# Optimization experiments

Hardware: AMD Instinct MI355X
Metric: run time of the kernel (lower is better)

Reference implementation:

```python
import jax, jax.numpy as jnp
import numpy as np

N_HEADS = 16
HEAD_DIM = 64  # dim=1024 / n_heads=16


def setup_inputs() -> dict:
    key = jax.random.key(0)
    ks = jax.random.split(key, 7)
    B, S, D = 4, 2048, 1024
    scale = 1.0 / np.sqrt(D)
    return {
        "q": jax.random.normal(ks[0], (B, S, D), jnp.float32),
        "k": jax.random.normal(ks[1], (B, S, D), jnp.float32),
        "v": jax.random.normal(ks[2], (B, S, D), jnp.float32),
        "Wq": jax.random.normal(ks[3], (D, D), jnp.float32) * scale,
        "Wk": jax.random.normal(ks[4], (D, D), jnp.float32) * scale,
        "Wv": jax.random.normal(ks[5], (D, D), jnp.float32) * scale,
        "Wo": jax.random.normal(ks[6], (D, D), jnp.float32) * scale,
    }


def reference(q, k, v, Wq, Wk, Wv, Wo):
    B, S, _ = q.shape
    H, Dh = N_HEADS, HEAD_DIM
    # linear projections (torch Linear: x @ W.T), reshape to [B, H, S, Dh]
    xq = (q @ Wq.T).reshape(B, S, H, Dh).transpose(0, 2, 1, 3)
    xk = (k @ Wk.T).reshape(B, S, H, Dh).transpose(0, 2, 1, 3)
    xv = (v @ Wv.T).reshape(B, S, H, Dh).transpose(0, 2, 1, 3)
    scores = jnp.einsum("bhsd,bhtd->bhst", xq, xk) / jnp.sqrt(jnp.float32(Dh))
    # causal mask: -inf above diagonal
    causal = jnp.triu(jnp.full((S, S), -jnp.inf, jnp.float32), k=1)
    scores = scores + causal[None, None]
    attn = jax.nn.softmax(scores.astype(jnp.float32), axis=-1).astype(xq.dtype)
    out = jnp.einsum("bhst,bhtd->bhsd", attn, xv)
    out = out.transpose(0, 2, 1, 3).reshape(B, S, H * Dh)
    return out @ Wo.T
```

## Files before the change

kernel.cpp:

```cpp
#include <hip/hip_runtime.h>
#include <hip/hip_bf16.h>

#define DI __device__ __forceinline__

typedef __attribute__((ext_vector_type(8))) short short8;
typedef __attribute__((ext_vector_type(4))) short short4v;
typedef __attribute__((ext_vector_type(4))) float f32x4;

#define QSCALE 0.180336885f

DI short f2bf(float f) {
  __hip_bfloat16 h = __float2bfloat16(f);
  return __builtin_bit_cast(short, h);
}

DI float fexp2(float x) {
#if __has_builtin(__builtin_amdgcn_exp2f)
  return __builtin_amdgcn_exp2f(x);
#else
  return exp2f(x);
#endif
}

DI void gl16(const short* g, short* l) {
  __builtin_amdgcn_global_load_lds(
      (const __attribute__((address_space(1))) void*)g,
      (__attribute__((address_space(3))) void*)l, 16, 0, 0);
}

__global__ __launch_bounds__(256) void convert_all(
    const float* __restrict__ q, const float* __restrict__ k,
    const float* __restrict__ v, const float* __restrict__ wq,
    const float* __restrict__ wk, const float* __restrict__ wv,
    const float* __restrict__ wo, short* __restrict__ qb,
    short* __restrict__ kb, short* __restrict__ vb, short* __restrict__ wb) {
  int z = blockIdx.z;
  const float* src;
  short* dst;
  if (z < 3) {
    src = (z == 0) ? q : (z == 1) ? k : v;
    dst = (z == 0) ? qb : (z == 1) ? kb : vb;
  } else {
    if (blockIdx.x >= 512) return;
    src = (z == 3) ? wq : (z == 4) ? wk : (z == 5) ? wv : wo;
    dst = wb + (size_t)(z - 3) * 1024 * 1024;
  }
  size_t i = ((size_t)blockIdx.x * 256 + threadIdx.x) * 8;
  float4 f0 = *(const float4*)(src + i);
  float4 f1 = *(const float4*)(src + i + 4);
  short8 o;
  o[0] = f2bf(f0.x); o[1] = f2bf(f0.y); o[2] = f2bf(f0.z); o[3] = f2bf(f0.w);
  o[4] = f2bf(f1.x); o[5] = f2bf(f1.y); o[6] = f2bf(f1.z); o[7] = f2bf(f1.w);
  *(short8*)(dst + i) = o;
}

__global__ __launch_bounds__(256) void convert_one(
    const float* __restrict__ src, short* __restrict__ dst) {
  size_t i = ((size_t)blockIdx.x * 256 + threadIdx.x) * 8;
  float4 f0 = *(const float4*)(src + i);
  float4 f1 = *(const float4*)(src + i + 4);
  short8 o;
  o[0] = f2bf(f0.x); o[1] = f2bf(f0.y); o[2] = f2bf(f0.z); o[3] = f2bf(f0.w);
  o[4] = f2bf(f1.x); o[5] = f2bf(f1.y); o[6] = f2bf(f1.z); o[7] = f2bf(f1.w);
  *(short8*)(dst + i) = o;
}

enum { OUT_F32 = 0, OUT_HEAD = 1, OUT_HEADT = 2 };

DI void stage_tile(const short* __restrict__ A, const short* __restrict__ B,
                   short* dA, short* dB, int bm, int bn, int k0, int wid,
                   int lrr, int lch) {
#pragma unroll
  for (int i = 0; i < 4; ++i) {
    int r0 = wid * 32 + i * 8;
    int rr = r0 + lrr;
    int sc = (lch ^ (rr & 7)) << 3;
    gl16(A + (size_t)(bm + rr) * 1024 + k0 + sc, dA + r0 * 64);
    gl16(B + (size_t)(bn + rr) * 1024 + k0 + sc, dB + r0 * 64);
  }
}

template <int OMODE>
DI void gemm_core(short* sA, short* sB, const short* __restrict__ A,
                  const short* __restrict__ B, void* __restrict__ Cp,
                  float scale, int bm, int bn) {
  const int tid = threadIdx.x;
  const int lane = tid & 63;
  const int wid = tid >> 6;
  const int wm = wid >> 1, wn = wid & 1;
  const int l15 = lane & 15, lq = lane >> 4;
  const int lrr = lane >> 3;
  const int lch = lane & 7;

  f32x4 acc[4][4] = {};

  stage_tile(A, B, sA, sB, bm, bn, 0, wid, lrr, lch);
  __syncthreads();

  int cur = 0;
  for (int t = 0; t < 16; ++t) {
    if (t + 1 < 16)
      stage_tile(A, B, sA + (cur ^ 1) * 8192, sB + (cur ^ 1) * 8192, bm, bn,
                 (t + 1) * 64, wid, lrr, lch);

    const char* bA = (const char*)(sA + cur * 8192);
    const char* bB = (const char*)(sB + cur * 8192);
#pragma unroll
    for (int ks = 0; ks < 2; ++ks) {
      short8 a[4], b[4];
#pragma unroll
      for (int mt = 0; mt < 4; ++mt) {
        int row = wm * 64 + mt * 16 + l15;
        int off = (row * 128 + ks * 64 + lq * 16) ^ ((row & 7) << 4);
        a[mt] = *(const short8*)(bA + off);
      }
#pragma unroll
      for (int nt = 0; nt < 4; ++nt) {
        int row = wn * 64 + nt * 16 + l15;
        int off = (row * 128 + ks * 64 + lq * 16) ^ ((row & 7) << 4);
        b[nt] = *(const short8*)(bB + off);
      }
#pragma unroll
      for (int mt = 0; mt < 4; ++mt)
#pragma unroll
        for (int nt = 0; nt < 4; ++nt) {
          if (OMODE == OUT_HEADT)
            acc[mt][nt] = __builtin_amdgcn_mfma_f32_16x16x32_bf16(
                b[nt], a[mt], acc[mt][nt], 0, 0, 0);
          else
            acc[mt][nt] = __builtin_amdgcn_mfma_f32_16x16x32_bf16(
                a[mt], b[nt], acc[mt][nt], 0, 0, 0);
        }
    }
    __syncthreads();
    cur ^= 1;
  }

#pragma unroll
  for (int mt = 0; mt < 4; ++mt) {
#pragma unroll
    for (int nt = 0; nt < 4; ++nt) {
#pragma unroll
      for (int r = 0; r < 4; ++r) {
        float val = acc[mt][nt][r] * scale;
        if (OMODE == OUT_HEADT) {
          int f = bn + wn * 64 + nt * 16 + lq * 4 + r;
          int t = bm + wm * 64 + mt * 16 + l15;
          int bb = t >> 11, s = t & 2047;
          int h = f >> 6, dh = f & 63;
          ((short*)Cp)[((size_t)((bb * 16 + h) * 64 + dh)) * 2048 + s] = f2bf(val);
        } else {
          int rowg = bm + wm * 64 + mt * 16 + lq * 4 + r;
          int colg = bn + wn * 64 + nt * 16 + l15;
          if (OMODE == OUT_HEAD) {
            int bb = rowg >> 11, s = rowg & 2047;
            int h = colg >> 6, dh = colg & 63;
            ((short*)Cp)[((size_t)(bb * 16 + h) * 2048 + s) * 64 + dh] = f2bf(val);
          } else {
            ((float*)Cp)[(size_t)rowg * 1024 + colg] = val;
          }
        }
      }
    }
  }
}

DI void xcd_map(int id, int& bm, int& bn) {
  int xcd = id & 7, slot = id >> 3;
  int panel = xcd + 8 * (slot >> 3);
  int ntile = slot & 7;
  bm = panel * 128;
  bn = ntile * 128;
}

#define GEMM_LDS()                                  \
  __shared__ __align__(16) short sA[2 * 128 * 64];  \
  __shared__ __align__(16) short sB[2 * 128 * 64];

__global__ __launch_bounds__(256) void proj_gemm3(
    const short* __restrict__ qb, const short* __restrict__ kb,
    const short* __restrict__ vb, const short* __restrict__ wq,
    const short* __restrict__ wk, const short* __restrict__ wv,
    short* __restrict__ xq, short* __restrict__ xk, short* __restrict__ xvT) {
  GEMM_LDS();
  int z = blockIdx.z;
  int bm, bn;
  xcd_map(blockIdx.x, bm, bn);
  if (z == 0) {
    gemm_core<OUT_HEAD>(sA, sB, qb, wq, xq, QSCALE, bm, bn);
  } else if (z == 1) {
    gemm_core<OUT_HEAD>(sA, sB, kb, wk, xk, 1.0f, bm, bn);
  } else {
    gemm_core<OUT_HEADT>(sA, sB, vb, wv, xvT, 1.0f, bm, bn);
  }
}

__global__ __launch_bounds__(256) void proj_oneN(
    const short* __restrict__ A, const short* __restrict__ B,
    short* __restrict__ C, float scale) {
  GEMM_LDS();
  int bm, bn;
  xcd_map(blockIdx.x, bm, bn);
  gemm_core<OUT_HEAD>(sA, sB, A, B, C, scale, bm, bn);
}

__global__ __launch_bounds__(256) void proj_oneT(
    const short* __restrict__ A, const short* __restrict__ B,
    short* __restrict__ C, float scale) {
  GEMM_LDS();
  int bm, bn;
  xcd_map(blockIdx.x, bm, bn);
  gemm_core<OUT_HEADT>(sA, sB, A, B, C, scale, bm, bn);
}

__global__ __launch_bounds__(256) void final_gemm(
    const short* __restrict__ oa, const short* __restrict__ wo,
    float* __restrict__ out) {
  GEMM_LDS();
  int bm, bn;
  xcd_map(blockIdx.x, bm, bn);
  gemm_core<OUT_F32>(sA, sB, oa, wo, out, 1.0f, bm, bn);
}

__global__ __launch_bounds__(512, 4) void attn_k(
    const short* __restrict__ Xq, const short* __restrict__ Xk,
    const short* __restrict__ XvT, short* __restrict__ Oa) {
  __shared__ __align__(16) short sK[2][64 * 64];
  __shared__ __align__(16) short sVT[2][64 * 64];
  __shared__ __align__(16) short sP[8][16 * 64];

  const int tid = threadIdx.x;
  const int lane = tid & 63;
  const int wid = tid >> 6;
  const int l15 = lane & 15, lq = lane >> 4;
  const int bid = blockIdx.x;
  const int ipair = bid >> 6;
  const int bh = bid & 63;
  const int b = bh >> 4, h = bh & 15;

  const short* Q = Xq + (size_t)bh * 2048 * 64;
  const short* K = Xk + (size_t)bh * 2048 * 64;
  const short* VT = XvT + (size_t)bh * 64 * 2048;

  const int srow = tid >> 3;
  const int scol = (tid & 7) * 8;
  const int soff = (srow * 128 + scol * 2) ^ ((srow & 7) << 4);

  short8 kreg, vreg;
  kreg = *(const short8*)(K + (size_t)srow * 64 + scol);
  vreg = *(const short8*)(VT + (size_t)srow * 2048 + scol);

  *(short8*)((char*)sK[0] + soff) = kreg;
  *(short8*)((char*)sVT[0] + soff) = vreg;

  short* sPw = sP[wid];
  int p = 0;

  for (int seg = 0; seg < 2; ++seg) {
    const int qt = seg ? ipair : (15 - ipair);
    const int qfirst = qt * 128 + wid * 16;
    const int qg = qfirst + l15;
    const int qlast = qfirst + 15;
    const int ntile = 2 * qt + 2;

    short8 qf[2];
#pragma unroll
    for (int ks = 0; ks < 2; ++ks)
      qf[ks] = *(const short8*)(Q + (size_t)qg * 64 + ks * 32 + lq * 8);

    float m_run = -1e30f, l_run = 0.f;
    f32x4 acc[4] = {};

    for (int kt = 0; kt < ntile; ++kt) {
      const int kv0 = kt * 64;
      __syncthreads();

      int nkt = kt + 1, nseg = seg;
      if (nkt >= ntile) { nseg = seg + 1; nkt = 0; }
      const bool hn = (nseg < 2);
      if (hn) {
        const int kn = nkt * 64;
        kreg = *(const short8*)(K + (size_t)(kn + srow) * 64 + scol);
        vreg = *(const short8*)(VT + (size_t)srow * 2048 + kn + scol);
      }

      const bool fullmask = (kv0 > qlast);
      if (!fullmask) {
        const bool needmask = (kv0 + 63 > qfirst);
        const char* bufK = (const char*)sK[p];
        const char* bufV = (const char*)sVT[p];

        f32x4 sc[4] = {};
        __builtin_amdgcn_s_setprio(1);
#pragma unroll
        for (int ks = 0; ks < 2; ++ks) {
          short8 kf[4];
#pragma unroll
          for (int nt = 0; nt < 4; ++nt) {
            int row = nt * 16 + l15;
            int off = (row * 128 + ks * 64 + lq * 16) ^ ((row & 7) << 4);
            kf[nt] = *(const short8*)(bufK + off);
          }
#pragma unroll
          for (int nt = 0; nt < 4; ++nt)
            sc[nt] = __builtin_amdgcn_mfma_f32_16x16x32_bf16(kf[nt], qf[ks],
                                                             sc[nt], 0, 0, 0);
        }
        __builtin_amdgcn_s_setprio(0);

        float pv[4][4];
        float m = -1e30f;
        if (needmask) {
#pragma unroll
          for (int nt = 0; nt < 4; ++nt)
#pragma unroll
            for (int r = 0; r < 4; ++r) {
              float s = sc[nt][r];
              if (kv0 + nt * 16 + lq * 4 + r > qg) s = -1e30f;
              pv[nt][r] = s;
              m = fmaxf(m, s);
            }
        } else {
#pragma unroll
          for (int nt = 0; nt < 4; ++nt)
#pragma unroll
            for (int r = 0; r < 4; ++r) {
              float s = sc[nt][r];
              pv[nt][r] = s;
              m = fmaxf(m, s);
            }
        }
        m = fmaxf(m, __shfl_xor(m, 16));
        m = fmaxf(m, __shfl_xor(m, 32));

        if (!__all(m - m_run <= 8.0f)) {
          const float m_new = fmaxf(m_run, m);
          const float corr = fexp2(m_run - m_new);
          l_run *= corr;
#pragma unroll
          for (int mt = 0; mt < 4; ++mt)
#pragma unroll
            for (int r = 0; r < 4; ++r) acc[mt][r] *= corr;
          m_run = m_new;
        }

        float rsum = 0.f;
#pragma unroll
        for (int nt = 0; nt < 4; ++nt)
#pragma unroll
          for (int r = 0; r < 4; ++r) {
            float e = fexp2(pv[nt][r] - m_run);
            pv[nt][r] = e;
            rsum += e;
          }
        rsum += __shfl_xor(rsum, 16);
        rsum += __shfl_xor(rsum, 32);
        l_run += rsum;

#pragma unroll
        for (int nt = 0; nt < 4; ++nt) {
          short4v pw;
#pragma unroll
          for (int r = 0; r < 4; ++r) pw[r] = f2bf(pv[nt][r]);
          int off = (l15 * 128 + nt * 32 + lq * 8) ^ ((l15 & 7) << 4);
          *(short4v*)((char*)sPw + off) = pw;
        }

        __builtin_amdgcn_s_setprio(1);
#pragma unroll
        for (int ks = 0; ks < 2; ++ks) {
          int poff = (l15 * 128 + ks * 64 + lq * 16) ^ ((l15 & 7) << 4);
          short8 pf = *(const short8*)((const char*)sPw + poff);
#pragma unroll
          for (int mt = 0; mt < 4; ++mt) {
            int row = mt * 16 + l15;
            int voff = (row * 128 + ks * 64 + lq * 16) ^ ((row & 7) << 4);
            short8 vf = *(const short8*)(bufV + voff);
            acc[mt] = __builtin_amdgcn_mfma_f32_16x16x32_bf16(vf, pf, acc[mt],
                                                              0, 0, 0);
          }
        }
        __builtin_amdgcn_s_setprio(0);
      }

      if (hn) {
        *(short8*)((char*)sK[p ^ 1] + soff) = kreg;
        *(short8*)((char*)sVT[p ^ 1] + soff) = vreg;
      }
      p ^= 1;
    }

    const float rl = 1.0f / l_run;
    short* orow = Oa + ((size_t)(b * 2048 + qg)) * 1024 + h * 64;
#pragma unroll
    for (int mt = 0; mt < 4; ++mt) {
      short4v o;
#pragma unroll
      for (int r = 0; r < 4; ++r) o[r] = f2bf(acc[mt][r] * rl);
      *(short4v*)(orow + mt * 16 + lq * 4) = o;
    }
  }
}

extern "C" void kernel_launch(void* const* d_in, const int* in_sizes, int n_in,
                              void* d_out, int out_size, void* d_ws,
                              size_t ws_size, hipStream_t stream) {
  const float* q = (const float*)d_in[0];
  const float* k = (const float*)d_in[1];
  const float* v = (const float*)d_in[2];
  const float* Wq = (const float*)d_in[3];
  const float* Wk = (const float*)d_in[4];
  const float* Wv = (const float*)d_in[5];
  const float* Wo = (const float*)d_in[6];

  char* ws = (char*)d_ws;
  short* wq_b = (short*)(ws + (0ull << 20));
  short* wk_b = (short*)(ws + (2ull << 20));
  short* wv_b = (short*)(ws + (4ull << 20));
  short* wo_b = (short*)(ws + (6ull << 20));
  short* xq  = (short*)(ws + (8ull << 20));
  short* xk  = (short*)(ws + (24ull << 20));
  short* xvT = (short*)(ws + (56ull << 20));

  if (ws_size >= (122ull << 20)) {
    short* qb = (short*)(ws + (72ull << 20));
    short* kb = (short*)(ws + (88ull << 20));
    short* vb = (short*)(ws + (104ull << 20));
    short* oa = qb;

    convert_all<<<dim3(4096, 1, 7), 256, 0, stream>>>(q, k, v, Wq, Wk, Wv, Wo,
                                                      qb, kb, vb, wq_b);
    proj_gemm3<<<dim3(512, 1, 3), 256, 0, stream>>>(qb, kb, vb, wq_b, wk_b,
                                                    wv_b, xq, xk, xvT);
    attn_k<<<dim3(512), 512, 0, stream>>>(xq, xk, xvT, oa);
    final_gemm<<<dim3(512), 256, 0, stream>>>(oa, wo_b, (float*)d_out);
  } else {
    short* X = (short*)(ws + (8ull << 20));
    short* xq2 = (short*)(ws + (24ull << 20));
    short* xk2 = (short*)(ws + (40ull << 20));
    short* xvT2 = (short*)(ws + (56ull << 20));
    short* oa2 = (short*)(ws + (72ull << 20));

    convert_one<<<dim3(512, 1, 4), 256, 0, stream>>>(Wq, wq_b);
    convert_one<<<dim3(512), 256, 0, stream>>>(Wk, wk_b);
    convert_one<<<dim3(512), 256, 0, stream>>>(Wv, wv_b);
    convert_one<<<dim3(512), 256, 0, stream>>>(Wo, wo_b);
    convert_one<<<dim3(4096), 256, 0, stream>>>(q, X);
    proj_oneN<<<dim3(512), 256, 0, stream>>>(X, wq_b, xq2, QSCALE);
    convert_one<<<dim3(4096), 256, 0, stream>>>(k, X);
    proj_oneN<<<dim3(512), 256, 0, stream>>>(X, wk_b, xk2, 1.0f);
    convert_one<<<dim3(4096), 256, 0, stream>>>(v, X);
    proj_oneT<<<dim3(512), 256, 0, stream>>>(X, wv_b, xvT2, 1.0f);
    attn_k<<<dim3(512), 512, 0, stream>>>(xq2, xk2, xvT2, oa2);
    final_gemm<<<dim3(512), 256, 0, stream>>>(oa2, wo_b, (float*)d_out);
  }
}
```

Measured before the change: 176.6 us.

## Fuse fp32-to-bf16 activation conversion into projection GEMM A-tile loading

The projection GEMM now reads fp32 q/k/v directly. It converts them to bf16 in registers and writes them into swizzled LDS, so the separate conversion pass over the activations is gone. That removes a full write and re-read of about 48MB of bf16 intermediates. In exchange, A-tile staging uses register-held global loads with conversion after the MFMA loop instead of async global_load_lds, which adds register pressure and may overlap loads with compute less well. The workspace-size fallback path is also removed.

```diff
diff --git a/kernel.cpp b/kernel.cpp
--- a/kernel.cpp
+++ b/kernel.cpp
@@ -28,23 +28,13 @@
       (__attribute__((address_space(3))) void*)l, 16, 0, 0);
 }
 
-__global__ __launch_bounds__(256) void convert_all(
-    const float* __restrict__ q, const float* __restrict__ k,
-    const float* __restrict__ v, const float* __restrict__ wq,
-    const float* __restrict__ wk, const float* __restrict__ wv,
-    const float* __restrict__ wo, short* __restrict__ qb,
-    short* __restrict__ kb, short* __restrict__ vb, short* __restrict__ wb) {
+__global__ __launch_bounds__(256) void convert_w4(
+    const float* __restrict__ wq, const float* __restrict__ wk,
+    const float* __restrict__ wv, const float* __restrict__ wo,
+    short* __restrict__ wb) {
   int z = blockIdx.z;
-  const float* src;
-  short* dst;
-  if (z < 3) {
-    src = (z == 0) ? q : (z == 1) ? k : v;
-    dst = (z == 0) ? qb : (z == 1) ? kb : vb;
-  } else {
-    if (blockIdx.x >= 512) return;
-    src = (z == 3) ? wq : (z == 4) ? wk : (z == 5) ? wv : wo;
-    dst = wb + (size_t)(z - 3) * 1024 * 1024;
-  }
+  const float* src = (z == 0) ? wq : (z == 1) ? wk : (z == 2) ? wv : wo;
+  short* dst = wb + (size_t)z * 1024 * 1024;
   size_t i = ((size_t)blockIdx.x * 256 + threadIdx.x) * 8;
   float4 f0 = *(const float4*)(src + i);
   float4 f1 = *(const float4*)(src + i + 4);
@@ -54,34 +44,32 @@
   *(short8*)(dst + i) = o;
 }
 
-__global__ __launch_bounds__(256) void convert_one(
-    const float* __restrict__ src, short* __restrict__ dst) {
-  size_t i = ((size_t)blockIdx.x * 256 + threadIdx.x) * 8;
-  float4 f0 = *(const float4*)(src + i);
-  float4 f1 = *(const float4*)(src + i + 4);
-  short8 o;
-  o[0] = f2bf(f0.x); o[1] = f2bf(f0.y); o[2] = f2bf(f0.z); o[3] = f2bf(f0.w);
-  o[4] = f2bf(f1.x); o[5] = f2bf(f1.y); o[6] = f2bf(f1.z); o[7] = f2bf(f1.w);
-  *(short8*)(dst + i) = o;
-}
-
 enum { OUT_F32 = 0, OUT_HEAD = 1, OUT_HEADT = 2 };
 
-DI void stage_tile(const short* __restrict__ A, const short* __restrict__ B,
-                   short* dA, short* dB, int bm, int bn, int k0, int wid,
-                   int lrr, int lch) {
+DI void stage_B(const short* __restrict__ B, short* dB, int bn, int k0,
+                int wid, int lrr, int lch) {
+#pragma unroll
+  for (int i = 0; i < 4; ++i) {
+    int r0 = wid * 32 + i * 8;
+    int rr = r0 + lrr;
+    int sc = (lch ^ (rr & 7)) << 3;
+    gl16(B + (size_t)(bn + rr) * 1024 + k0 + sc, dB + r0 * 64);
+  }
+}
+
+DI void stage_A16(const short* __restrict__ A, short* dA, int bm, int k0,
+                  int wid, int lrr, int lch) {
 #pragma unroll
   for (int i = 0; i < 4; ++i) {
     int r0 = wid * 32 + i * 8;
     int rr = r0 + lrr;
     int sc = (lch ^ (rr & 7)) << 3;
     gl16(A + (size_t)(bm + rr) * 1024 + k0 + sc, dA + r0 * 64);
-    gl16(B + (size_t)(bn + rr) * 1024 + k0 + sc, dB + r0 * 64);
-  }
-}
-
-template <int OMODE>
-DI void gemm_core(short* sA, short* sB, const short* __restrict__ A,
+  }
+}
+
+template <int OMODE, bool AF32>
+DI void gemm_core(short* sA, short* sB, const void* __restrict__ Ap,
                   const short* __restrict__ B, void* __restrict__ Cp,
                   float scale, int bm, int bn) {
   const int tid = threadIdx.x;
@@ -92,16 +80,59 @@
   const int lrr = lane >> 3;
   const int lch = lane & 7;
 
+  const float* Af = (const float*)Ap;
+  const short* Ab = (const short*)Ap;
+
   f32x4 acc[4][4] = {};
-
-  stage_tile(A, B, sA, sB, bm, bn, 0, wid, lrr, lch);
+  float4 fa[4][2];
+
+  if (AF32) {
+#pragma unroll
+    for (int t = 0; t < 4; ++t) {
+      int c = tid + t * 256;
+      int row = c >> 3, col = (c & 7) * 8;
+      const float* src = Af + (size_t)(bm + row) * 1024 + col;
+      fa[t][0] = *(const float4*)src;
+      fa[t][1] = *(const float4*)(src + 4);
+    }
+    stage_B(B, sB, bn, 0, wid, lrr, lch);
+#pragma unroll
+    for (int t = 0; t < 4; ++t) {
+      int c = tid + t * 256;
+      int row = c >> 3, col = (c & 7) * 8;
+      short8 vv;
+      vv[0] = f2bf(fa[t][0].x); vv[1] = f2bf(fa[t][0].y);
+      vv[2] = f2bf(fa[t][0].z); vv[3] = f2bf(fa[t][0].w);
+      vv[4] = f2bf(fa[t][1].x); vv[5] = f2bf(fa[t][1].y);
+      vv[6] = f2bf(fa[t][1].z); vv[7] = f2bf(fa[t][1].w);
+      int off = (row * 128 + col * 2) ^ ((row & 7) << 4);
+      *(short8*)((char*)sA + off) = vv;
+    }
+  } else {
+    stage_A16(Ab, sA, bm, 0, wid, lrr, lch);
+    stage_B(B, sB, bn, 0, wid, lrr, lch);
+  }
   __syncthreads();
 
   int cur = 0;
-  for (int t = 0; t < 16; ++t) {
-    if (t + 1 < 16)
-      stage_tile(A, B, sA + (cur ^ 1) * 8192, sB + (cur ^ 1) * 8192, bm, bn,
-                 (t + 1) * 64, wid, lrr, lch);
+  for (int t16 = 0; t16 < 16; ++t16) {
+    const bool more = (t16 + 1 < 16);
+    if (more) {
+      int k1 = (t16 + 1) * 64;
+      if (AF32) {
+#pragma unroll
+        for (int t = 0; t < 4; ++t) {
+          int c = tid + t * 256;
+          int row = c >> 3, col = (c & 7) * 8;
+          const float* src = Af + (size_t)(bm + row) * 1024 + k1 + col;
+          fa[t][0] = *(const float4*)src;
+          fa[t][1] = *(const float4*)(src + 4);
+        }
+      } else {
+        stage_A16(Ab, sA + (cur ^ 1) * 8192, bm, k1, wid, lrr, lch);
+      }
+      stage_B(B, sB + (cur ^ 1) * 8192, bn, k1, wid, lrr, lch);
+    }
 
     const char* bA = (const char*)(sA + cur * 8192);
     const char* bB = (const char*)(sB + cur * 8192);
@@ -131,6 +162,22 @@
             acc[mt][nt] = __builtin_amdgcn_mfma_f32_16x16x32_bf16(
                 a[mt], b[nt], acc[mt][nt], 0, 0, 0);
         }
+    }
+
+    if (AF32 && more) {
+      short* dA = sA + (cur ^ 1) * 8192;
+#pragma unroll
+      for (int t = 0; t < 4; ++t) {
+        int c = tid + t * 256;
+        int row = c >> 3, col = (c & 7) * 8;
+        short8 vv;
+        vv[0] = f2bf(fa[t][0].x); vv[1] = f2bf(fa[t][0].y);
+        vv[2] = f2bf(fa[t][0].z); vv[3] = f2bf(fa[t][0].w);
+        vv[4] = f2bf(fa[t][1].x); vv[5] = f2bf(fa[t][1].y);
+        vv[6] = f2bf(fa[t][1].z); vv[7] = f2bf(fa[t][1].w);
+        int off = (row * 128 + col * 2) ^ ((row & 7) << 4);
+        *(short8*)((char*)dA + off) = vv;
+      }
     }
     __syncthreads();
     cur ^= 1;
@@ -178,8 +225,8 @@
   __shared__ __align__(16) short sB[2 * 128 * 64];
 
 __global__ __launch_bounds__(256) void proj_gemm3(
-    const short* __restrict__ qb, const short* __restrict__ kb,
-    const short* __restrict__ vb, const short* __restrict__ wq,
+    const float* __restrict__ q, const float* __restrict__ k,
+    const float* __restrict__ v, const short* __restrict__ wq,
     const short* __restrict__ wk, const short* __restrict__ wv,
     short* __restrict__ xq, short* __restrict__ xk, short* __restrict__ xvT) {
   GEMM_LDS();
@@ -187,30 +234,12 @@
   int bm, bn;
   xcd_map(blockIdx.x, bm, bn);
   if (z == 0) {
-    gemm_core<OUT_HEAD>(sA, sB, qb, wq, xq, QSCALE, bm, bn);
+    gemm_core<OUT_HEAD, true>(sA, sB, q, wq, xq, QSCALE, bm, bn);
   } else if (z == 1) {
-    gemm_core<OUT_HEAD>(sA, sB, kb, wk, xk, 1.0f, bm, bn);
+    gemm_core<OUT_HEAD, true>(sA, sB, k, wk, xk, 1.0f, bm, bn);
   } else {
-    gemm_core<OUT_HEADT>(sA, sB, vb, wv, xvT, 1.0f, bm, bn);
-  }
-}
-
-__global__ __launch_bounds__(256) void proj_oneN(
-    const short* __restrict__ A, const short* __restrict__ B,
-    short* __restrict__ C, float scale) {
-  GEMM_LDS();
-  int bm, bn;
-  xcd_map(blockIdx.x, bm, bn);
-  gemm_core<OUT_HEAD>(sA, sB, A, B, C, scale, bm, bn);
-}
-
-__global__ __launch_bounds__(256) void proj_oneT(
-    const short* __restrict__ A, const short* __restrict__ B,
-    short* __restrict__ C, float scale) {
-  GEMM_LDS();
-  int bm, bn;
-  xcd_map(blockIdx.x, bm, bn);
-  gemm_core<OUT_HEADT>(sA, sB, A, B, C, scale, bm, bn);
+    gemm_core<OUT_HEADT, true>(sA, sB, v, wv, xvT, 1.0f, bm, bn);
+  }
 }
 
 __global__ __launch_bounds__(256) void final_gemm(
@@ -219,7 +248,7 @@
   GEMM_LDS();
   int bm, bn;
   xcd_map(blockIdx.x, bm, bn);
-  gemm_core<OUT_F32>(sA, sB, oa, wo, out, 1.0f, bm, bn);
+  gemm_core<OUT_F32, false>(sA, sB, oa, wo, out, 1.0f, bm, bn);
 }
 
 __global__ __launch_bounds__(512, 4) void attn_k(
@@ -420,38 +449,12 @@
   short* wo_b = (short*)(ws + (6ull << 20));
   short* xq  = (short*)(ws + (8ull << 20));
   short* xk  = (short*)(ws + (24ull << 20));
-  short* xvT = (short*)(ws + (56ull << 20));
-
-  if (ws_size >= (122ull << 20)) {
-    short* qb = (short*)(ws + (72ull << 20));
-    short* kb = (short*)(ws + (88ull << 20));
-    short* vb = (short*)(ws + (104ull << 20));
-    short* oa = qb;
-
-    convert_all<<<dim3(4096, 1, 7), 256, 0, stream>>>(q, k, v, Wq, Wk, Wv, Wo,
-                                                      qb, kb, vb, wq_b);
-    proj_gemm3<<<dim3(512, 1, 3), 256, 0, stream>>>(qb, kb, vb, wq_b, wk_b,
-                                                    wv_b, xq, xk, xvT);
-    attn_k<<<dim3(512), 512, 0, stream>>>(xq, xk, xvT, oa);
-    final_gemm<<<dim3(512), 256, 0, stream>>>(oa, wo_b, (float*)d_out);
-  } else {
-    short* X = (short*)(ws + (8ull << 20));
-    short* xq2 = (short*)(ws + (24ull << 20));
-    short* xk2 = (short*)(ws + (40ull << 20));
-    short* xvT2 = (short*)(ws + (56ull << 20));
-    short* oa2 = (short*)(ws + (72ull << 20));
-
-    convert_one<<<dim3(512, 1, 4), 256, 0, stream>>>(Wq, wq_b);
-    convert_one<<<dim3(512), 256, 0, stream>>>(Wk, wk_b);
-    convert_one<<<dim3(512), 256, 0, stream>>>(Wv, wv_b);
-    convert_one<<<dim3(512), 256, 0, stream>>>(Wo, wo_b);
-    convert_one<<<dim3(4096), 256, 0, stream>>>(q, X);
-    proj_oneN<<<dim3(512), 256, 0, stream>>>(X, wq_b, xq2, QSCALE);
-    convert_one<<<dim3(4096), 256, 0, stream>>>(k, X);
-    proj_oneN<<<dim3(512), 256, 0, stream>>>(X, wk_b, xk2, 1.0f);
-    convert_one<<<dim3(4096), 256, 0, stream>>>(v, X);
-    proj_oneT<<<dim3(512), 256, 0, stream>>>(X, wv_b, xvT2, 1.0f);
-    attn_k<<<dim3(512), 512, 0, stream>>>(xq2, xk2, xvT2, oa2);
-    final_gemm<<<dim3(512), 256, 0, stream>>>(oa2, wo_b, (float*)d_out);
-  }
-}
+  short* xvT = (short*)(ws + (40ull << 20));
+  short* oa  = (short*)(ws + (56ull << 20));
+
+  convert_w4<<<dim3(512, 1, 4), 256, 0, stream>>>(Wq, Wk, Wv, Wo, wq_b);
+  proj_gemm3<<<dim3(512, 1, 3), 256, 0, stream>>>(q, k, v, wq_b, wk_b, wv_b,
+                                                  xq, xk, xvT);
+  attn_k<<<dim3(512), 512, 0, stream>>>(xq, xk, xvT, oa);
+  final_gemm<<<dim3(512), 256, 0, stream>>>(oa, wo_b, (float*)d_out);
+}
```

Measured after the change: 188.4 us. 6.7% more time.

## Drop LDS double buffering, swap MFMA operands, vectorize GEMM epilogue stores

Applied to the files above, without the earlier changes.

Replaces the double-buffered LDS pipeline in the shared GEMM core with a single buffer that is loaded and then computed, with a barrier between the two phases. This halves LDS use per block, which may allow more resident blocks, but global loads no longer overlap the MFMAs. The MFMA operand order is swapped so each lane holds 4 contiguous output elements, which lets the epilogue write them as short4 or float4 vector stores instead of scalar stores. A convert_one launch in the fallback path also drops a redundant z dimension.

```diff
diff --git a/kernel.cpp b/kernel.cpp
--- a/kernel.cpp
+++ b/kernel.cpp
@@ -67,19 +67,6 @@
 
 enum { OUT_F32 = 0, OUT_HEAD = 1, OUT_HEADT = 2 };
 
-DI void stage_tile(const short* __restrict__ A, const short* __restrict__ B,
-                   short* dA, short* dB, int bm, int bn, int k0, int wid,
-                   int lrr, int lch) {
-#pragma unroll
-  for (int i = 0; i < 4; ++i) {
-    int r0 = wid * 32 + i * 8;
-    int rr = r0 + lrr;
-    int sc = (lch ^ (rr & 7)) << 3;
-    gl16(A + (size_t)(bm + rr) * 1024 + k0 + sc, dA + r0 * 64);
-    gl16(B + (size_t)(bn + rr) * 1024 + k0 + sc, dB + r0 * 64);
-  }
-}
-
 template <int OMODE>
 DI void gemm_core(short* sA, short* sB, const short* __restrict__ A,
                   const short* __restrict__ B, void* __restrict__ Cp,
@@ -94,17 +81,17 @@
 
   f32x4 acc[4][4] = {};
 
-  stage_tile(A, B, sA, sB, bm, bn, 0, wid, lrr, lch);
-  __syncthreads();
-
-  int cur = 0;
-  for (int t = 0; t < 16; ++t) {
-    if (t + 1 < 16)
-      stage_tile(A, B, sA + (cur ^ 1) * 8192, sB + (cur ^ 1) * 8192, bm, bn,
-                 (t + 1) * 64, wid, lrr, lch);
-
-    const char* bA = (const char*)(sA + cur * 8192);
-    const char* bB = (const char*)(sB + cur * 8192);
+  for (int k0 = 0; k0 < 1024; k0 += 64) {
+#pragma unroll
+    for (int i = 0; i < 4; ++i) {
+      int r0 = wid * 32 + i * 8;
+      int rr = r0 + lrr;
+      int sc = (lch ^ (rr & 7)) << 3;
+      gl16(A + (size_t)(bm + rr) * 1024 + k0 + sc, sA + r0 * 64);
+      gl16(B + (size_t)(bn + rr) * 1024 + k0 + sc, sB + r0 * 64);
+    }
+    __syncthreads();
+
 #pragma unroll
     for (int ks = 0; ks < 2; ++ks) {
       short8 a[4], b[4];
@@ -112,13 +99,13 @@
       for (int mt = 0; mt < 4; ++mt) {
         int row = wm * 64 + mt * 16 + l15;
         int off = (row * 128 + ks * 64 + lq * 16) ^ ((row & 7) << 4);
-        a[mt] = *(const short8*)(bA + off);
+        a[mt] = *(const short8*)((const char*)sA + off);
       }
 #pragma unroll
       for (int nt = 0; nt < 4; ++nt) {
         int row = wn * 64 + nt * 16 + l15;
         int off = (row * 128 + ks * 64 + lq * 16) ^ ((row & 7) << 4);
-        b[nt] = *(const short8*)(bB + off);
+        b[nt] = *(const short8*)((const char*)sB + off);
       }
 #pragma unroll
       for (int mt = 0; mt < 4; ++mt)
@@ -126,40 +113,48 @@
         for (int nt = 0; nt < 4; ++nt) {
           if (OMODE == OUT_HEADT)
             acc[mt][nt] = __builtin_amdgcn_mfma_f32_16x16x32_bf16(
-                b[nt], a[mt], acc[mt][nt], 0, 0, 0);
+                a[mt], b[nt], acc[mt][nt], 0, 0, 0);
           else
             acc[mt][nt] = __builtin_amdgcn_mfma_f32_16x16x32_bf16(
-                a[mt], b[nt], acc[mt][nt], 0, 0, 0);
+                b[nt], a[mt], acc[mt][nt], 0, 0, 0);
         }
     }
     __syncthreads();
-    cur ^= 1;
   }
 
 #pragma unroll
   for (int mt = 0; mt < 4; ++mt) {
 #pragma unroll
     for (int nt = 0; nt < 4; ++nt) {
-#pragma unroll
-      for (int r = 0; r < 4; ++r) {
-        float val = acc[mt][nt][r] * scale;
-        if (OMODE == OUT_HEADT) {
-          int f = bn + wn * 64 + nt * 16 + lq * 4 + r;
-          int t = bm + wm * 64 + mt * 16 + l15;
-          int bb = t >> 11, s = t & 2047;
-          int h = f >> 6, dh = f & 63;
-          ((short*)Cp)[((size_t)((bb * 16 + h) * 64 + dh)) * 2048 + s] = f2bf(val);
-        } else {
-          int rowg = bm + wm * 64 + mt * 16 + lq * 4 + r;
-          int colg = bn + wn * 64 + nt * 16 + l15;
-          if (OMODE == OUT_HEAD) {
-            int bb = rowg >> 11, s = rowg & 2047;
-            int h = colg >> 6, dh = colg & 63;
-            ((short*)Cp)[((size_t)(bb * 16 + h) * 2048 + s) * 64 + dh] = f2bf(val);
-          } else {
-            ((float*)Cp)[(size_t)rowg * 1024 + colg] = val;
-          }
-        }
+      if (OMODE == OUT_HEAD) {
+        int t = bm + wm * 64 + mt * 16 + l15;
+        int f0 = bn + wn * 64 + nt * 16 + lq * 4;
+        int bb = t >> 11, s = t & 2047;
+        int h = f0 >> 6, dh0 = f0 & 63;
+        short4v o;
+#pragma unroll
+        for (int r = 0; r < 4; ++r) o[r] = f2bf(acc[mt][nt][r] * scale);
+        *(short4v*)((short*)Cp + ((size_t)((bb * 16 + h) * 2048 + s)) * 64 +
+                    dh0) = o;
+      } else if (OMODE == OUT_F32) {
+        int t = bm + wm * 64 + mt * 16 + l15;
+        int f0 = bn + wn * 64 + nt * 16 + lq * 4;
+        float4 o;
+        o.x = acc[mt][nt][0] * scale;
+        o.y = acc[mt][nt][1] * scale;
+        o.z = acc[mt][nt][2] * scale;
+        o.w = acc[mt][nt][3] * scale;
+        *(float4*)((float*)Cp + (size_t)t * 1024 + f0) = o;
+      } else {
+        int t0 = bm + wm * 64 + mt * 16 + lq * 4;
+        int f = bn + wn * 64 + nt * 16 + l15;
+        int bb = t0 >> 11, s0 = t0 & 2047;
+        int h = f >> 6, dh = f & 63;
+        short4v o;
+#pragma unroll
+        for (int r = 0; r < 4; ++r) o[r] = f2bf(acc[mt][nt][r] * scale);
+        *(short4v*)((short*)Cp + ((size_t)((bb * 16 + h) * 64 + dh)) * 2048 +
+                    s0) = o;
       }
     }
   }
@@ -173,9 +168,9 @@
   bn = ntile * 128;
 }
 
-#define GEMM_LDS()                                  \
-  __shared__ __align__(16) short sA[2 * 128 * 64];  \
-  __shared__ __align__(16) short sB[2 * 128 * 64];
+#define GEMM_LDS()                              \
+  __shared__ __align__(16) short sA[128 * 64];  \
+  __shared__ __align__(16) short sB[128 * 64];
 
 __global__ __launch_bounds__(256) void proj_gemm3(
     const short* __restrict__ qb, const short* __restrict__ kb,
@@ -441,7 +436,7 @@
     short* xvT2 = (short*)(ws + (56ull << 20));
     short* oa2 = (short*)(ws + (72ull << 20));
 
-    convert_one<<<dim3(512, 1, 4), 256, 0, stream>>>(Wq, wq_b);
+    convert_one<<<dim3(512), 256, 0, stream>>>(Wq, wq_b);
     convert_one<<<dim3(512), 256, 0, stream>>>(Wk, wk_b);
     convert_one<<<dim3(512), 256, 0, stream>>>(Wv, wv_b);
     convert_one<<<dim3(512), 256, 0, stream>>>(Wo, wo_b);
```

Measured after the change: 180.3 us. 2.1% more time.
